# Optimization experiments

Measured on AMD Instinct MI355X. Metric: run time of the kernel, lower is better.

The kernel has to match this reference:

```python
import jax, jax.numpy as jnp
from jax import lax
import numpy as np

B, H, W, C = 8, 128, 128, 256
NUM_ANCHORS_PER_LOC = 15  # len(scales)=5 * len(ratios)=3


def _conv(x, w, b, padding):
    # NHWC conv, HWIO kernel (matches keras Conv2D)
    y = lax.conv_general_dilated(x, w, window_strides=(1, 1), padding=padding,
                                 dimension_numbers=('NHWC', 'HWIO', 'NHWC'))
    return y + b


def setup_inputs() -> dict:
    key = jax.random.key(0)
    ks = jax.random.split(key, 5)
    std = jnp.float32(0.01)  # TruncatedNormal(0, 0.01) init in original
    x = jax.random.normal(ks[0], (B, H, W, C), jnp.float32)
    w_shared = jax.random.normal(ks[1], (3, 3, C, 512), jnp.float32) * std
    b_shared = jnp.zeros((512,), jnp.float32)
    w_cls = jax.random.normal(ks[2], (1, 1, 512, 2 * NUM_ANCHORS_PER_LOC), jnp.float32) * std
    b_cls = jnp.zeros((2 * NUM_ANCHORS_PER_LOC,), jnp.float32)
    w_reg = jax.random.normal(ks[3], (1, 1, 512, 4 * NUM_ANCHORS_PER_LOC), jnp.float32) * std
    b_reg = jnp.zeros((4 * NUM_ANCHORS_PER_LOC,), jnp.float32)
    return {'x': x, 'w_shared': w_shared, 'b_shared': b_shared,
            'w_cls': w_cls, 'b_cls': b_cls, 'w_reg': w_reg, 'b_reg': b_reg}


def reference(x, w_shared, b_shared, w_cls, b_cls, w_reg, b_reg):
    # shared 3x3 conv + relu6
    shared = jnp.clip(_conv(x, w_shared, b_shared, 'SAME'), 0.0, 6.0)
    # class branch: 1x1 conv -> [B, num_anchors, 2] -> softmax
    cls = _conv(shared, w_cls, b_cls, 'VALID')
    rpn_class_logits = cls.reshape(cls.shape[0], -1, 2)
    rpn_probs = jax.nn.softmax(rpn_class_logits, axis=-1)
    reg = _conv(shared, w_reg, b_reg, 'VALID')
    rpn_deltas = reg.reshape(reg.shape[0], -1, 4)
    return (rpn_class_logits, rpn_probs, rpn_deltas)
```

## Files before the change

### kernel.cpp

```cpp
#include <hip/hip_runtime.h>
#include <stdint.h>


#define HH 128
#define WW 128
#define CIN 256

typedef __attribute__((ext_vector_type(8))) short short8;
typedef __attribute__((ext_vector_type(4))) float f32x4;

#define LDS_B_OFF 66560
#define LDS_TOTAL 132096

static __device__ __forceinline__ unsigned short f2bf(float f) {
    uint32_t u = __float_as_uint(f);
    uint32_t r = (u + 0x7FFFu + ((u >> 16) & 1u)) >> 16;
    return (unsigned short)r;
}

__global__ __launch_bounds__(256) void prep_wk(const float* __restrict__ w,
                                               unsigned short* __restrict__ wk) {
    int t = blockIdx.x * 256 + threadIdx.x;
    int c_idx = t >> 15;
    int r = t & 32767;
    int n = r >> 6, kk = r & 63;
    int dydx = c_idx >> 2, kc = c_idx & 3;
    int k = kc * 64 + kk;
    float v = w[((size_t)(dydx * 256 + k)) * 512 + n];
    int sw = (((kk * 2) ^ ((n & 7) << 4)) >> 1);
    wk[(size_t)c_idx * 32768 + n * 64 + sw] = f2bf(v);
}

__global__ __launch_bounds__(256) void prep_wbr(const float* __restrict__ wc,
                                                const float* __restrict__ wr,
                                                unsigned short* __restrict__ wbr) {
    int t = blockIdx.x * 256 + threadIdx.x;
    int n = t >> 9, k = t & 511;
    float v = 0.f;
    if (n < 30) v = wc[k * 30 + n];
    else if (n >= 32 && n < 92) v = wr[k * 60 + (n - 32)];
    wbr[n * 512 + k] = f2bf(v);
}

__global__ __launch_bounds__(512) void rpn_fused(
    const float* __restrict__ x, const unsigned short* __restrict__ wk,
    const float* __restrict__ bsh, const unsigned short* __restrict__ wbr,
    const float* __restrict__ bcls, const float* __restrict__ breg,
    float* __restrict__ out)
{
    extern __shared__ char smem[];
    const int tid = threadIdx.x;
    const int lane = tid & 63;
    const int wid = tid >> 6;
    const int wm = wid >> 2, wn = wid & 3;
    const int l15 = lane & 15, l4 = lane >> 4;
    const int blk = blockIdx.x;
    const int bb = blk >> 7, h = blk & 127;

    f32x4 acc[4][8];
    #pragma unroll
    for (int i = 0; i < 4; ++i)
        #pragma unroll
        for (int j = 0; j < 8; ++j) acc[i][j] = (f32x4){0.f, 0.f, 0.f, 0.f};

    for (int dy = 0; dy < 3; ++dy) {
        __syncthreads();
        {
            const int hp = h + dy - 1;
            const bool hin = (hp >= 0) && (hp < HH);
            const float* xrow = x + ((size_t)(bb * HH + hp)) * WW * CIN;
            for (int u = tid; u < 130 * 32; u += 512) {
                const int pos = u >> 5, c8 = u & 31;
                const int wc = pos - 1;
                float4 f0 = make_float4(0.f,0.f,0.f,0.f), f1 = make_float4(0.f,0.f,0.f,0.f);
                if (hin && (unsigned)wc < WW) {
                    const float4* p = reinterpret_cast<const float4*>(xrow + (size_t)wc * CIN + c8 * 8);
                    f0 = p[0]; f1 = p[1];
                }
                short8 v;
                v[0]=(short)f2bf(f0.x); v[1]=(short)f2bf(f0.y);
                v[2]=(short)f2bf(f0.z); v[3]=(short)f2bf(f0.w);
                v[4]=(short)f2bf(f1.x); v[5]=(short)f2bf(f1.y);
                v[6]=(short)f2bf(f1.z); v[7]=(short)f2bf(f1.w);
                *reinterpret_cast<short8*>(smem + pos * 512 + ((c8 * 16) ^ ((pos & 7) << 4))) = v;
            }
        }
        for (int dx = 0; dx < 3; ++dx) {
            const int dydx = dy * 3 + dx;
            for (int kc = 0; kc < 4; ++kc) {
                if (!(dx == 0 && kc == 0)) __syncthreads();
                {
                    const char* src = reinterpret_cast<const char*>(wk)
                                    + ((size_t)(dydx * 4 + kc)) * 65536 + tid * 16;
                    char* dst = smem + LDS_B_OFF + tid * 16;
                    #pragma unroll
                    for (int i = 0; i < 8; ++i) {
                        __builtin_amdgcn_global_load_lds(
                            reinterpret_cast<const uint32_t*>(src + i * 8192),
                            reinterpret_cast<uint32_t*>(dst + i * 8192), 16, 0, 0);
                    }
                }
                __syncthreads();
                #pragma unroll
                for (int ks = 0; ks < 2; ++ks) {
                    short8 af[4];
                    const int ch = kc * 64 + ks * 32 + l4 * 8;
                    #pragma unroll
                    for (int mf = 0; mf < 4; ++mf) {
                        const int row = wm * 64 + mf * 16 + l15 + dx;
                        af[mf] = *reinterpret_cast<const short8*>(
                            smem + row * 512 + ((ch * 2) ^ ((row & 7) << 4)));
                    }
                    const int kk = ks * 32 + l4 * 8;
                    #pragma unroll
                    for (int nf = 0; nf < 8; ++nf) {
                        const int n = wn * 128 + nf * 16 + l15;
                        short8 bf = *reinterpret_cast<const short8*>(
                            smem + LDS_B_OFF + n * 128 + ((kk * 2) ^ ((n & 7) << 4)));
                        #pragma unroll
                        for (int mf = 0; mf < 4; ++mf)
                            acc[mf][nf] = __builtin_amdgcn_mfma_f32_16x16x32_bf16(
                                af[mf], bf, acc[mf][nf], 0, 0, 0);
                    }
                }
            }
        }
    }

    __syncthreads();
    #pragma unroll
    for (int nf = 0; nf < 8; ++nf) {
        const int ch = wn * 128 + nf * 16 + l15;
        const float bv = bsh[ch];
        #pragma unroll
        for (int mf = 0; mf < 4; ++mf) {
            #pragma unroll
            for (int r = 0; r < 4; ++r) {
                const int pos = wm * 64 + mf * 16 + l4 * 4 + r;
                float v = acc[mf][nf][r] + bv;
                v = fminf(fmaxf(v, 0.f), 6.f);
                *reinterpret_cast<unsigned short*>(
                    smem + pos * 1024 + ((ch * 2) ^ ((pos & 7) << 4))) = f2bf(v);
            }
        }
    }
    __syncthreads();

    f32x4 bacc[6];
    #pragma unroll
    for (int nf = 0; nf < 6; ++nf) bacc[nf] = (f32x4){0.f,0.f,0.f,0.f};
    const int pos0 = wid * 16;
    #pragma unroll 4
    for (int kstep = 0; kstep < 16; ++kstep) {
        const int ch = kstep * 32 + l4 * 8;
        const int posr = pos0 + l15;
        short8 af = *reinterpret_cast<const short8*>(
            smem + posr * 1024 + ((ch * 2) ^ ((posr & 7) << 4)));
        #pragma unroll
        for (int nf = 0; nf < 6; ++nf) {
            const int n = nf * 16 + l15;
            short8 bfr = *reinterpret_cast<const short8*>(wbr + n * 512 + ch);
            bacc[nf] = __builtin_amdgcn_mfma_f32_16x16x32_bf16(af, bfr, bacc[nf], 0, 0, 0);
        }
    }

    const size_t rowbase = (size_t)h * 128;
    #pragma unroll
    for (int nf = 0; nf < 2; ++nf) {
        const int n = nf * 16 + l15;
        const float bias = (n < 30) ? bcls[n] : 0.f;
        #pragma unroll
        for (int r = 0; r < 4; ++r) {
            float v = bacc[nf][r] + bias;
            float vo = __shfl_xor(v, 1);
            float mx = fmaxf(v, vo);
            float e  = __expf(v - mx), eo = __expf(vo - mx);
            float p  = e / (e + eo);
            if (n < 30) {
                const int wc = pos0 + l4 * 4 + r;
                const size_t anchor = (rowbase + wc) * 15 + (n >> 1);
                const size_t idx = (size_t)bb * 491520 + anchor * 2 + (n & 1);
                out[idx] = v;
                out[3932160 + idx] = p;
            }
        }
    }
    #pragma unroll
    for (int nf = 2; nf < 6; ++nf) {
        const int n = nf * 16 + l15;
        const int nr = n - 32;
        const float bias = (nr < 60) ? breg[nr] : 0.f;
        #pragma unroll
        for (int r = 0; r < 4; ++r) {
            float v = bacc[nf][r] + bias;
            if (nr < 60) {
                const int wc = pos0 + l4 * 4 + r;
                const size_t anchor = (rowbase + wc) * 15 + (nr >> 2);
                out[7864320 + (size_t)bb * 983040 + anchor * 4 + (nr & 3)] = v;
            }
        }
    }
}

extern "C" void kernel_launch(void* const* d_in, const int* in_sizes, int n_in,
                              void* d_out, int out_size, void* d_ws, size_t ws_size,
                              hipStream_t stream) {
    const float* x    = (const float*)d_in[0];
    const float* wsh  = (const float*)d_in[1];
    const float* bsh  = (const float*)d_in[2];
    const float* wcls = (const float*)d_in[3];
    const float* bcls = (const float*)d_in[4];
    const float* wreg = (const float*)d_in[5];
    const float* breg = (const float*)d_in[6];
    float* out = (float*)d_out;

    unsigned short* wk  = (unsigned short*)d_ws;
    unsigned short* wbr = wk + 1179648;

    prep_wk <<<4608, 256, 0, stream>>>(wsh, wk);
    prep_wbr<<<192, 256, 0, stream>>>(wcls, wreg, wbr);

    hipFuncSetAttribute((const void*)rpn_fused,
                        hipFuncAttributeMaxDynamicSharedMemorySize, LDS_TOTAL);
    rpn_fused<<<1024, 512, LDS_TOTAL, stream>>>(x, wk, bsh, wbr, bcls, breg, out);
}
```

Measured before the change: 649.1 us.

## Double-buffer weight tiles with async LDS prefetch and tiled weight transpose

Splits the weight stream into 32-wide K chunks that are double-buffered in LDS. The next chunk is prefetched with global_load_lds while the MFMAs of the current chunk run, using manual waitcnt and raw barriers in place of the two __syncthreads per chunk. The weight prep kernel now transposes through a shared-memory tile to get coalesced reads, and the unswizzled B layout is read directly. The main kernel also gets a two-blocks-per-SM launch bound and setprio around the MFMA burst. The hand-written waitcnt and barrier sequencing is fragile and could race if the counts are wrong.

```diff
diff --git a/kernel.cpp b/kernel.cpp
--- a/kernel.cpp
+++ b/kernel.cpp
@@ -20,15 +20,23 @@
 
 __global__ __launch_bounds__(256) void prep_wk(const float* __restrict__ w,
                                                unsigned short* __restrict__ wk) {
-    int t = blockIdx.x * 256 + threadIdx.x;
-    int c_idx = t >> 15;
-    int r = t & 32767;
-    int n = r >> 6, kk = r & 63;
-    int dydx = c_idx >> 2, kc = c_idx & 3;
-    int k = kc * 64 + kk;
-    float v = w[((size_t)(dydx * 256 + k)) * 512 + n];
-    int sw = (((kk * 2) ^ ((n & 7) << 4)) >> 1);
-    wk[(size_t)c_idx * 32768 + n * 64 + sw] = f2bf(v);
+    __shared__ unsigned short t[32][130];
+    const int c = blockIdx.x >> 2, nh = blockIdx.x & 3;
+    const int dydx = c >> 3, kc = c & 7;
+    #pragma unroll
+    for (int e = 0; e < 16; ++e) {
+        int idx = e * 256 + threadIdx.x;
+        int kk = idx >> 7, n0 = idx & 127;
+        float v = w[((size_t)(dydx * 256 + kc * 32 + kk)) * 512 + nh * 128 + n0];
+        t[kk][n0] = f2bf(v);
+    }
+    __syncthreads();
+    #pragma unroll
+    for (int e = 0; e < 16; ++e) {
+        int idx = e * 256 + threadIdx.x;
+        int n0 = idx >> 5, kk = idx & 31;
+        wk[(size_t)c * 16384 + (size_t)(nh * 128 + n0) * 32 + kk] = t[kk][n0];
+    }
 }
 
 __global__ __launch_bounds__(256) void prep_wbr(const float* __restrict__ wc,
@@ -42,7 +50,7 @@
     wbr[n * 512 + k] = f2bf(v);
 }
 
-__global__ __launch_bounds__(512) void rpn_fused(
+__global__ __launch_bounds__(512, 2) void rpn_fused(
     const float* __restrict__ x, const unsigned short* __restrict__ wk,
     const float* __restrict__ bsh, const unsigned short* __restrict__ wbr,
     const float* __restrict__ bcls, const float* __restrict__ breg,
@@ -63,8 +71,18 @@
         #pragma unroll
         for (int j = 0; j < 8; ++j) acc[i][j] = (f32x4){0.f, 0.f, 0.f, 0.f};
 
+    {
+        const char* src = reinterpret_cast<const char*>(wk) + tid * 16;
+        char* dst = smem + LDS_B_OFF + tid * 16;
+        #pragma unroll
+        for (int r = 0; r < 4; ++r)
+            __builtin_amdgcn_global_load_lds(
+                reinterpret_cast<const uint32_t*>(src + r * 8192),
+                reinterpret_cast<uint32_t*>(dst + r * 8192), 16, 0, 0);
+    }
+
+    int g = 0;
     for (int dy = 0; dy < 3; ++dy) {
-        __syncthreads();
         {
             const int hp = h + dy - 1;
             const bool hin = (hp >= 0) && (hp < HH);
@@ -85,45 +103,53 @@
                 *reinterpret_cast<short8*>(smem + pos * 512 + ((c8 * 16) ^ ((pos & 7) << 4))) = v;
             }
         }
-        for (int dx = 0; dx < 3; ++dx) {
-            const int dydx = dy * 3 + dx;
-            for (int kc = 0; kc < 4; ++kc) {
-                if (!(dx == 0 && kc == 0)) __syncthreads();
-                {
-                    const char* src = reinterpret_cast<const char*>(wk)
-                                    + ((size_t)(dydx * 4 + kc)) * 65536 + tid * 16;
-                    char* dst = smem + LDS_B_OFF + tid * 16;
-                    #pragma unroll
-                    for (int i = 0; i < 8; ++i) {
-                        __builtin_amdgcn_global_load_lds(
-                            reinterpret_cast<const uint32_t*>(src + i * 8192),
-                            reinterpret_cast<uint32_t*>(dst + i * 8192), 16, 0, 0);
-                    }
-                }
-                __syncthreads();
+        for (int i = 0; i < 24; ++i, ++g) {
+            const int nxt = g + 1;
+            if (nxt < 72) {
+                const char* src = reinterpret_cast<const char*>(wk) + (size_t)nxt * 32768 + tid * 16;
+                char* dst = smem + LDS_B_OFF + ((nxt & 1) << 15) + tid * 16;
                 #pragma unroll
-                for (int ks = 0; ks < 2; ++ks) {
-                    short8 af[4];
-                    const int ch = kc * 64 + ks * 32 + l4 * 8;
-                    #pragma unroll
-                    for (int mf = 0; mf < 4; ++mf) {
-                        const int row = wm * 64 + mf * 16 + l15 + dx;
-                        af[mf] = *reinterpret_cast<const short8*>(
-                            smem + row * 512 + ((ch * 2) ^ ((row & 7) << 4)));
-                    }
-                    const int kk = ks * 32 + l4 * 8;
-                    #pragma unroll
-                    for (int nf = 0; nf < 8; ++nf) {
-                        const int n = wn * 128 + nf * 16 + l15;
-                        short8 bf = *reinterpret_cast<const short8*>(
-                            smem + LDS_B_OFF + n * 128 + ((kk * 2) ^ ((n & 7) << 4)));
-                        #pragma unroll
-                        for (int mf = 0; mf < 4; ++mf)
-                            acc[mf][nf] = __builtin_amdgcn_mfma_f32_16x16x32_bf16(
-                                af[mf], bf, acc[mf][nf], 0, 0, 0);
-                    }
-                }
-            }
+                for (int r = 0; r < 4; ++r)
+                    __builtin_amdgcn_global_load_lds(
+                        reinterpret_cast<const uint32_t*>(src + r * 8192),
+                        reinterpret_cast<uint32_t*>(dst + r * 8192), 16, 0, 0);
+                if (i == 0) asm volatile("s_waitcnt vmcnt(4) lgkmcnt(0)" ::: "memory");
+                else        asm volatile("s_waitcnt vmcnt(4)" ::: "memory");
+            } else {
+                asm volatile("s_waitcnt vmcnt(0) lgkmcnt(0)" ::: "memory");
+            }
+            __builtin_amdgcn_s_barrier();
+            asm volatile("" ::: "memory");
+
+            const int dx = (g >> 3) % 3;
+            const int kc = g & 7;
+            const char* bbuf = smem + LDS_B_OFF + ((g & 1) << 15);
+
+            short8 af[4];
+            const int ch = kc * 32 + l4 * 8;
+            #pragma unroll
+            for (int mf = 0; mf < 4; ++mf) {
+                const int row = wm * 64 + mf * 16 + l15 + dx;
+                af[mf] = *reinterpret_cast<const short8*>(
+                    smem + row * 512 + ((ch * 2) ^ ((row & 7) << 4)));
+            }
+            short8 bf[8];
+            #pragma unroll
+            for (int nf = 0; nf < 8; ++nf) {
+                const int n = wn * 128 + nf * 16 + l15;
+                bf[nf] = *reinterpret_cast<const short8*>(bbuf + n * 64 + l4 * 16);
+            }
+            asm volatile("s_waitcnt lgkmcnt(0)" ::: "memory");
+            __builtin_amdgcn_s_setprio(1);
+            #pragma unroll
+            for (int nf = 0; nf < 8; ++nf)
+                #pragma unroll
+                for (int mf = 0; mf < 4; ++mf)
+                    acc[mf][nf] = __builtin_amdgcn_mfma_f32_16x16x32_bf16(
+                        af[mf], bf[nf], acc[mf][nf], 0, 0, 0);
+            __builtin_amdgcn_s_setprio(0);
+            __builtin_amdgcn_s_barrier();
+            asm volatile("" ::: "memory");
         }
     }
 
@@ -217,7 +243,7 @@
     unsigned short* wk  = (unsigned short*)d_ws;
     unsigned short* wbr = wk + 1179648;
 
-    prep_wk <<<4608, 256, 0, stream>>>(wsh, wk);
+    prep_wk <<<288, 256, 0, stream>>>(wsh, wk);
     prep_wbr<<<192, 256, 0, stream>>>(wcls, wreg, wbr);
 
     hipFuncSetAttribute((const void*)rpn_fused,
```

Result: faster. 616.0 us (-5.1%).
